# Optimization experiments

Measured on AMD Instinct MI355X. Metric: run time of the kernel, lower is better.

The kernel has to match this reference:

```python
import jax, jax.numpy as jnp
import numpy as np


def lut_quantize(v, lut):
    """Nearest-neighbor LUT quantization with straight-through estimator.
    lut is sorted ascending; uses searchsorted (no [N, L] blowup)."""
    L = lut.shape[0]
    idx = jnp.clip(jnp.searchsorted(lut, v), 1, L - 1)
    left = jnp.take(lut, idx - 1)
    right = jnp.take(lut, idx)
    q = jnp.where(v - left <= right - v, left, right)
    return v + jax.lax.stop_gradient(q - v)


def mem_conv(x, w, b, lut):
    # memConv2d: weights/bias snapped to LUT levels, then standard 3x3 SAME conv (NCHW/OIHW)
    wq = lut_quantize(w, lut)
    bq = lut_quantize(b, lut)
    y = jax.lax.conv_general_dilated(x, wq, window_strides=(1, 1),
                                     padding=((1, 1), (1, 1)),
                                     dimension_numbers=('NCHW', 'OIHW', 'NCHW'))
    return y + bq[None, :, None, None]


def mem_linear(x, w, b, lut):
    # memLinear: torch-style weight (out, in)
    return x @ lut_quantize(w, lut).T + lut_quantize(b, lut)


def mem_relu(x, lut):
    # memReLu: ReLU followed by LUT quantization of the activation
    return lut_quantize(jnp.maximum(x, 0.0), lut)


def max_pool_2x2(x):
    return jax.lax.reduce_window(x, -jnp.inf, jax.lax.max,
                                 (1, 1, 2, 2), (1, 1, 2, 2), 'VALID')


def _forward(x, lut, w1, b1, w2, b2, w3, b3, w4, b4, w5, b5, w6, b6,
             fw1, fb1, fw2, fb2, fw3, fb3):
    x = mem_relu(mem_conv(x, w1, b1, lut), lut)
    x = mem_relu(mem_conv(x, w2, b2, lut), lut)
    x = max_pool_2x2(x)                      # [B,32,16,16]
    x = mem_relu(mem_conv(x, w3, b3, lut), lut)
    x = mem_relu(mem_conv(x, w4, b4, lut), lut)
    x = max_pool_2x2(x)                      # [B,64,8,8]
    x = mem_relu(mem_conv(x, w5, b5, lut), lut)
    x = mem_relu(mem_conv(x, w6, b6, lut), lut)
    x = max_pool_2x2(x)                      # [B,128,4,4]
    x = x.reshape(-1, 128 * 4 * 4)
    x = mem_relu(mem_linear(x, fw1, fb1, lut), lut)
    x = mem_relu(mem_linear(x, fw2, fb2, lut), lut)
    x = mem_linear(x, fw3, fb3, lut)
    return jax.nn.softmax(x, axis=1)


def setup_inputs() -> dict:
    key = jax.random.key(0)
    ks = jax.random.split(key, 20)
    B = 512
    lut = jnp.linspace(-4.0, 4.0, 129).astype(jnp.float32)

    def conv_w(k, co, ci):
        scale = np.sqrt(2.0 / (ci * 9)).astype(np.float32)
        return jax.random.normal(k, (co, ci, 3, 3), jnp.float32) * scale

    def lin_w(k, co, ci):
        scale = np.sqrt(2.0 / ci).astype(np.float32)
        return jax.random.normal(k, (co, ci), jnp.float32) * scale

    return {
        'x': jax.random.normal(ks[0], (B, 3, 32, 32), jnp.float32),
        'lut': lut,
        'w1': conv_w(ks[1], 32, 3),   'b1': jnp.zeros((32,), jnp.float32),
        'w2': conv_w(ks[2], 32, 32),  'b2': jnp.zeros((32,), jnp.float32),
        'w3': conv_w(ks[3], 64, 32),  'b3': jnp.zeros((64,), jnp.float32),
        'w4': conv_w(ks[4], 64, 64),  'b4': jnp.zeros((64,), jnp.float32),
        'w5': conv_w(ks[5], 128, 64), 'b5': jnp.zeros((128,), jnp.float32),
        'w6': conv_w(ks[6], 128, 128),'b6': jnp.zeros((128,), jnp.float32),
        'fw1': lin_w(ks[7], 512, 2048), 'fb1': jnp.zeros((512,), jnp.float32),
        'fw2': lin_w(ks[8], 128, 512),  'fb2': jnp.zeros((128,), jnp.float32),
        'fw3': lin_w(ks[9], 10, 128),   'fb3': jnp.zeros((10,), jnp.float32),
    }


def reference(x, lut, w1, b1, w2, b2, w3, b3, w4, b4, w5, b5, w6, b6,
              fw1, fb1, fw2, fb2, fw3, fb3):
    return _forward(x, lut, w1, b1, w2, b2, w3, b3, w4, b4, w5, b5, w6, b6,
                    fw1, fb1, fw2, fb2, fw3, fb3)
```

## Files before the change

### kernel.cpp

```cpp
#include <hip/hip_runtime.h>
#include <cstddef>


#define B_SZ 512
typedef unsigned int u32;
typedef __attribute__((ext_vector_type(4))) int i32x4;

__device__ __forceinline__ float lutq(float v) {
    float k = ceilf(v * 16.0f - 0.5f);
    k = fminf(64.0f, fmaxf(-64.0f, k));
    return k * 0.0625f;
}
__device__ __forceinline__ int kq(float x) {
    float kf = ceilf(x * 16.0f - 0.5f);
    kf = fminf(64.0f, fmaxf(-64.0f, kf));
    return (int)kf;
}
__device__ __forceinline__ u32 bmax4u(u32 a, u32 b) {
    u32 r = 0;
    #pragma unroll
    for (int j = 0; j < 4; ++j) {
        u32 x = (a >> (8 * j)) & 255u, y = (b >> (8 * j)) & 255u;
        r |= (x > y ? x : y) << (8 * j);
    }
    return r;
}

__device__ __forceinline__ void prep_conv_frag(const float* __restrict__ w, char* __restrict__ q,
                                               int i, int CI) {
    int NSTEP = (9 * CI + 63) / 64;
    int e = i & 15, t = i >> 4;
    int ln = t & 63, t2 = t >> 6;
    int s = t2 % NSTEP, co_tile = t2 / NSTEP;
    int k = s * 64 + ((ln >> 4) << 4) + e;
    int tap = k / CI, ci = k % CI;
    int co = co_tile * 16 + (ln & 15);
    int val = 0;
    if (tap < 9) val = kq(w[(co * CI + ci) * 9 + tap]);
    q[i] = (char)val;
}
__device__ __forceinline__ void prep_fc_frag(const float* __restrict__ w, char* __restrict__ q,
                                             int i, int K) {
    int S = K >> 6;
    int e = i & 15, t = i >> 4;
    int ln = t & 63, t2 = t >> 6;
    int s = t2 % S, n_tile = t2 / S;
    int n = n_tile * 16 + (ln & 15);
    int k = s * 64 + ((ln >> 4) << 4) + e;
    q[i] = (char)kq(w[(size_t)n * K + k]);
}

__global__ __launch_bounds__(256) void prep_conv1(
    const float* __restrict__ w2, const float* __restrict__ w3, const float* __restrict__ w4,
    const float* __restrict__ w5, const float* __restrict__ w6,
    const float* __restrict__ fw1, const float* __restrict__ fw2,
    char* q2, char* q3, char* q4, char* q5, char* q6, char* qf1, char* qf2,
    const float* __restrict__ x, const float* __restrict__ w1,
    const float* __restrict__ b1, char* __restrict__ out)
{
    const int tid = threadIdx.x;
    const int bid = blockIdx.x;
    if (bid < 5480) {
        int i = bid * 256 + tid;
        if (i < 10240)                  { prep_conv_frag(w2, q2, i, 32);  }
        else if ((i -= 10240) < 20480)  { prep_conv_frag(w3, q3, i, 32);  }
        else if ((i -= 20480) < 36864)  { prep_conv_frag(w4, q4, i, 64);  }
        else if ((i -= 36864) < 73728)  { prep_conv_frag(w5, q5, i, 64);  }
        else if ((i -= 73728) < 147456) { prep_conv_frag(w6, q6, i, 128); }
        else if ((i -= 147456) < 1048576){ prep_fc_frag(fw1, qf1, i, 2048); }
        else if ((i -= 1048576) < 65536) { prep_fc_frag(fw2, qf2, i, 512);  }
        return;
    }
    __shared__ float s_w[3][9][32];
    __shared__ float s_b[32];
    __shared__ float s_in[3][10][34];
    const int bx  = bid - 5480;
    const int b   = bx >> 2;
    const int r0  = (bx & 3) * 8;
    for (int i = tid; i < 864; i += 256) {
        int o = i % 32, k = (i / 32) % 9, c = i / 288;
        s_w[c][k][o] = lutq(w1[(o * 3 + c) * 9 + k]);
    }
    if (tid < 32) s_b[tid] = lutq(b1[tid]);
    for (int i = tid; i < 3 * 10 * 34; i += 256) {
        int xx = i % 34, yy = (i / 34) % 10, c = i / 340;
        int gy = r0 + yy - 1, gx = xx - 1;
        float v = 0.f;
        if ((unsigned)gy < 32u && (unsigned)gx < 32u)
            v = x[(((size_t)b * 3 + c) * 32 + gy) * 32 + gx];
        s_in[c][yy][xx] = v;
    }
    __syncthreads();
    const int y = tid >> 5, xx = tid & 31;
    float acc[32];
    #pragma unroll
    for (int o = 0; o < 32; ++o) acc[o] = 0.f;
    #pragma unroll
    for (int c = 0; c < 3; ++c) {
        #pragma unroll
        for (int k = 0; k < 9; ++k) {
            float iv = s_in[c][y + k / 3][xx + k % 3];
            #pragma unroll
            for (int o = 0; o < 32; ++o) acc[o] = fmaf(iv, s_w[c][k][o], acc[o]);
        }
    }
    u32 u[8];
    #pragma unroll
    for (int j = 0; j < 8; ++j) {
        u32 p = 0;
        #pragma unroll
        for (int q = 0; q < 4; ++q) {
            float v = fmaxf(acc[4 * j + q] + s_b[4 * j + q], 0.f);
            int kk = (int)ceilf(v * 16.0f - 0.5f);
            kk = kk > 64 ? 64 : kk;
            p |= ((u32)kk & 255u) << (8 * q);
        }
        u[j] = p;
    }
    const int p = (b << 10) + ((r0 + y) << 5) + xx;
    u32* o4 = (u32*)(out + (size_t)p * 32);
    #pragma unroll
    for (int j = 0; j < 8; ++j) o4[j] = u[j];
}

template<int HW, int CI, int CO, int RS, int NIMG, int NT, int POOL = 0>
__global__ __launch_bounds__(256) void conv_mfma(
    const char* __restrict__ in,
    const char* __restrict__ wq,
    const float* __restrict__ bias,
    char* __restrict__ out)
{
    constexpr int PH  = HW + 2;
    constexpr int PIX = NIMG * (RS + 2) * PH;
    constexpr int M   = NIMG * RS * HW;
    constexpr int MT  = M / 16;
    constexpr int MW  = MT / 4;
    constexpr int NSTEP = (9 * CI + 63) / 64;
    constexpr int SL  = HW / RS;
    constexpr int NC16 = CI / 16;
    constexpr int NTC = NT * 16;

    __shared__ __align__(128) char s_in[PIX * CI];

    const int tid = threadIdx.x;
    const int g   = blockIdx.x;
    const int b0  = (g / SL) * NIMG;
    const int r0  = (g % SL) * RS;
    const int co0 = blockIdx.y * NTC;

    constexpr int TOTC = PIX * NC16;
    for (int i = tid; i < TOTC; i += 256) {
        int c16 = i % NC16;
        int pp  = i / NC16;
        int xx  = pp % PH;
        int rr  = pp / PH;
        int yy  = rr % (RS + 2);
        int img = rr / (RS + 2);
        int gy = r0 + yy - 1, gx = xx - 1;
        uint4 v = {0u, 0u, 0u, 0u};
        if ((unsigned)gy < (unsigned)HW && (unsigned)gx < (unsigned)HW)
            v = *(const uint4*)(in + ((((size_t)(b0 + img) * HW + gy) * HW + gx) * CI + c16 * 16));
        int off = (pp * CI + c16 * 16) ^ ((pp & 7) << 4);
        *(uint4*)(s_in + off) = v;
    }
    __syncthreads();

    const int wv = tid >> 6, ln = tid & 63;
    const int l15 = ln & 15, lq = ln >> 4;

    int ppad[MW];
    #pragma unroll
    for (int mw = 0; mw < MW; ++mw) {
        int p = (wv * MW + mw) * 16 + l15;
        int img = p / (RS * HW);
        int rem = p % (RS * HW);
        int ly = rem / HW, lx = rem % HW;
        ppad[mw] = (img * (RS + 2) + ly + 1) * PH + lx + 1;
    }

    i32x4 acc[MW][NT] = {};

    const char* wtile = wq + ((size_t)blockIdx.y * NT) * NSTEP * 1024 + (ln << 4);
    auto dp = [](int t) { return (t / 3 - 1) * PH + (t % 3 - 1); };

    #pragma unroll
    for (int s = 0; s < NSTEP; ++s) {
        i32x4 bf[NT];
        #pragma unroll
        for (int nt = 0; nt < NT; ++nt)
            bf[nt] = *(const i32x4*)(wtile + ((nt * NSTEP + s) << 10));
        int dd, ci0;
        if constexpr (CI == 32) {
            int d0 = dp(2 * s);
            int d1 = (2 * s + 1 < 9) ? dp(2 * s + 1) : 0;
            dd  = (lq & 2) ? d1 : d0;
            ci0 = (lq & 1) << 4;
        } else if constexpr (CI == 64) {
            dd  = dp(s);
            ci0 = lq << 4;
        } else {
            dd  = dp(s >> 1);
            ci0 = ((s & 1) << 6) + (lq << 4);
        }
        #pragma unroll
        for (int mw = 0; mw < MW; ++mw) {
            int pix = ppad[mw] + dd;
            int off = (pix * CI + ci0) ^ ((pix & 7) << 4);
            i32x4 af = *(const i32x4*)(s_in + off);
            #pragma unroll
            for (int nt = 0; nt < NT; ++nt)
                acc[mw][nt] = __builtin_amdgcn_mfma_i32_16x16x64_i8(af, bf[nt], acc[mw][nt], 0, 0, 0);
        }
    }

    if constexpr (POOL == 0) {
        #pragma unroll
        for (int nt = 0; nt < NT; ++nt) {
            int kb16 = 16 * kq(bias[co0 + nt * 16 + l15]);
            #pragma unroll
            for (int mw = 0; mw < MW; ++mw) {
                #pragma unroll
                for (int r = 0; r < 4; ++r) {
                    int p = (wv * MW + mw) * 16 + lq * 4 + r;
                    int img = p / (RS * HW), rem = p % (RS * HW);
                    int ly = rem / HW, lx = rem % HW;
                    int vv = acc[mw][nt][r] + kb16;
                    vv = vv > 0 ? vv : 0;
                    int kk = (vv + 7) >> 4;
                    kk = kk > 64 ? 64 : kk;
                    out[(((size_t)(b0 + img) * HW + r0 + ly) * HW + lx) * CO + co0 + nt * 16 + l15] = (char)kk;
                }
            }
        }
    } else {
        __syncthreads();
        char* s_out = s_in;
        #pragma unroll
        for (int nt = 0; nt < NT; ++nt) {
            int kb16 = 16 * kq(bias[co0 + nt * 16 + l15]);
            #pragma unroll
            for (int mw = 0; mw < MW; ++mw) {
                #pragma unroll
                for (int r = 0; r < 4; ++r) {
                    int p = (wv * MW + mw) * 16 + lq * 4 + r;
                    int vv = acc[mw][nt][r] + kb16;
                    vv = vv > 0 ? vv : 0;
                    int kk = (vv + 7) >> 4;
                    kk = kk > 64 ? 64 : kk;
                    s_out[p * NTC + nt * 16 + l15] = (char)kk;
                }
            }
        }
        __syncthreads();
        constexpr int PR = RS / 2, PC = HW / 2, HOW = HW / 2;
        constexpr int OCT = NIMG * PR * PC * (NTC / 16);
        for (int idx = tid; idx < OCT; idx += 256) {
            int c16 = idx % (NTC / 16);
            int pp  = idx / (NTC / 16);
            int xo = pp % PC, yo = (pp / PC) % PR, img = pp / (PC * PR);
            int pb = (img * RS + 2 * yo) * HW + 2 * xo;
            uint4 v0 = *(const uint4*)(s_out + (pb)          * NTC + c16 * 16);
            uint4 v1 = *(const uint4*)(s_out + (pb + 1)      * NTC + c16 * 16);
            uint4 v2 = *(const uint4*)(s_out + (pb + HW)     * NTC + c16 * 16);
            uint4 v3 = *(const uint4*)(s_out + (pb + HW + 1) * NTC + c16 * 16);
            uint4 r;
            r.x = bmax4u(bmax4u(v0.x, v1.x), bmax4u(v2.x, v3.x));
            r.y = bmax4u(bmax4u(v0.y, v1.y), bmax4u(v2.y, v3.y));
            r.z = bmax4u(bmax4u(v0.z, v1.z), bmax4u(v2.z, v3.z));
            r.w = bmax4u(bmax4u(v0.w, v1.w), bmax4u(v2.w, v3.w));
            if constexpr (POOL == 1) {
                *(uint4*)(out + ((((size_t)(b0 + img) * HOW + (r0 >> 1) + yo) * HOW + xo) * CO
                                 + co0 + c16 * 16)) = r;
            } else {
                const char* rv = (const char*)&r;
                int m = b0 + img;
                #pragma unroll
                for (int j = 0; j < 16; ++j) {
                    int c = co0 + c16 * 16 + j;
                    int k = c * 16 + yo * 4 + xo;
                    int off = (((m >> 4) * 32 + (k >> 6)) << 10)
                            + ((((k >> 4) & 3) * 16 + (m & 15)) << 4) + (k & 15);
                    out[off] = rv[j];
                }
            }
        }
    }
}

template<int N, int K, int SK>
__global__ __launch_bounds__(256) void fc1_splitk(
    const char* __restrict__ xa, const char* __restrict__ wq, int* __restrict__ part)
{
    constexpr int KCH = K / SK;
    constexpr int KS = K / 64;
    const int tid = threadIdx.x, wv = tid >> 6, ln = tid & 63;
    const int l15 = ln & 15, lq = ln >> 4;
    const int m0 = blockIdx.x * 128, n0 = blockIdx.y * 128;
    const int kb = blockIdx.z * KCH;
    const int mq = (wv >> 1) * 4, nq = (wv & 1) * 4;
    i32x4 acc[4][4] = {};
    const char* xr[4];
    const char* wt[4];
    #pragma unroll
    for (int t = 0; t < 4; ++t) {
        xr[t] = xa + (size_t)((m0 >> 4) + mq + t) * KS * 1024 + (ln << 4);
        wt[t] = wq + (size_t)((n0 >> 4) + nq + t) * KS * 1024 + (ln << 4);
    }
    for (int k0 = 0; k0 < KCH; k0 += 64) {
        const int s = (kb + k0) >> 6;
        i32x4 a[4], b[4];
        #pragma unroll
        for (int t = 0; t < 4; ++t) {
            a[t] = *(const i32x4*)(xr[t] + (s << 10));
            b[t] = *(const i32x4*)(wt[t] + (s << 10));
        }
        #pragma unroll
        for (int i = 0; i < 4; ++i)
            #pragma unroll
            for (int j = 0; j < 4; ++j)
                acc[i][j] = __builtin_amdgcn_mfma_i32_16x16x64_i8(a[i], b[j], acc[i][j], 0, 0, 0);
    }
    int* pb = part + (size_t)blockIdx.z * (B_SZ * N);
    #pragma unroll
    for (int j = 0; j < 4; ++j) {
        int n = n0 + (nq + j) * 16 + l15;
        #pragma unroll
        for (int i = 0; i < 4; ++i)
            #pragma unroll
            for (int r = 0; r < 4; ++r) {
                int m = m0 + (mq + i) * 16 + lq * 4 + r;
                pb[(size_t)m * N + n] = acc[i][j][r];
            }
    }
}

template<int N, int SK>
__global__ __launch_bounds__(256) void fc_reduce(
    const int* __restrict__ part, const float* __restrict__ bias, char* __restrict__ out)
{
    int i = blockIdx.x * 256 + threadIdx.x;
    if (i >= B_SZ * N) return;
    int s = 0;
    #pragma unroll
    for (int k = 0; k < SK; ++k) s += part[(size_t)k * (B_SZ * N) + i];
    int vv = s + 16 * kq(bias[i % N]);
    vv = vv > 0 ? vv : 0;
    int kk = (vv + 7) >> 4;
    kk = kk > 64 ? 64 : kk;
    out[i] = (char)kk;
}

__global__ __launch_bounds__(256) void fc_tail(
    const char* __restrict__ x, const char* __restrict__ qf2,
    const float* __restrict__ fb2, const float* __restrict__ fw3,
    const float* __restrict__ fb3, float* __restrict__ out)
{
    __shared__ __align__(16) char sx[16 * 512];
    __shared__ __align__(16) char sy[16 * 128];
    __shared__ __align__(16) char sw3[10 * 128];
    __shared__ float sb3[10];
    __shared__ int sp[16][16][10];

    const int tid = threadIdx.x;
    const int m0 = blockIdx.x * 16;

    for (int idx = tid; idx < 512; idx += 256) {
        int r = idx >> 5, c16 = idx & 31;
        uint4 v = *(const uint4*)(x + (size_t)(m0 + r) * 512 + c16 * 16);
        *(uint4*)(sx + ((r * 512 + c16 * 16) ^ ((r & 7) << 4))) = v;
    }
    for (int i = tid; i < 1280; i += 256) sw3[i] = (char)kq(fw3[i]);
    if (tid < 10) sb3[tid] = lutq(fb3[tid]);
    __syncthreads();

    const int wv = tid >> 6, ln = tid & 63, l15 = ln & 15, lq = ln >> 4;
    const int ntg = wv * 2;
    i32x4 acc[2] = {};
    #pragma unroll
    for (int s = 0; s < 8; ++s) {
        int row = l15;
        i32x4 a = *(const i32x4*)(sx + ((row * 512 + s * 64 + lq * 16) ^ ((row & 7) << 4)));
        #pragma unroll
        for (int nt = 0; nt < 2; ++nt) {
            i32x4 b = *(const i32x4*)(qf2 + (((ntg + nt) * 8 + s) << 10) + (ln << 4));
            acc[nt] = __builtin_amdgcn_mfma_i32_16x16x64_i8(a, b, acc[nt], 0, 0, 0);
        }
    }
    #pragma unroll
    for (int nt = 0; nt < 2; ++nt) {
        int n = (ntg + nt) * 16 + l15;
        int kb16 = 16 * kq(fb2[n]);
        #pragma unroll
        for (int r = 0; r < 4; ++r) {
            int row = lq * 4 + r;
            int vv = acc[nt][r] + kb16;
            vv = vv > 0 ? vv : 0;
            int kk = (vv + 7) >> 4;
            kk = kk > 64 ? 64 : kk;
            sy[(row * 128 + n) ^ ((row & 7) << 4)] = (char)kk;
        }
    }
    __syncthreads();

    {
        int r = tid >> 4, g = tid & 15;
        uint2 yv = *(const uint2*)(sy + ((r * 128 + g * 8) ^ ((r & 7) << 4)));
        const char* yb = (const char*)&yv;
        #pragma unroll
        for (int o = 0; o < 10; ++o) {
            uint2 wv2 = *(const uint2*)(sw3 + o * 128 + g * 8);
            const char* wb = (const char*)&wv2;
            int S = 0;
            #pragma unroll
            for (int e = 0; e < 8; ++e) S += (int)yb[e] * (int)wb[e];
            sp[r][g][o] = S;
        }
    }
    __syncthreads();

    if (tid < 16) {
        int r = tid;
        float d[10];
        #pragma unroll
        for (int o = 0; o < 10; ++o) {
            int S = 0;
            #pragma unroll
            for (int g = 0; g < 16; ++g) S += sp[r][g][o];
            d[o] = (float)S * 0.00390625f + sb3[o];
        }
        float m = d[0];
        #pragma unroll
        for (int o = 1; o < 10; ++o) m = fmaxf(m, d[o]);
        float e[10];
        float sum = 0.f;
        #pragma unroll
        for (int o = 0; o < 10; ++o) { e[o] = expf(d[o] - m); sum += e[o]; }
        #pragma unroll
        for (int o = 0; o < 10; ++o) out[(size_t)(m0 + r) * 10 + o] = e[o] / sum;
    }
}

extern "C" void kernel_launch(void* const* d_in, const int* in_sizes, int n_in,
                              void* d_out, int out_size, void* d_ws, size_t ws_size,
                              hipStream_t stream)
{
    const float* x   = (const float*)d_in[0];
    const float* w1  = (const float*)d_in[2];
    const float* b1  = (const float*)d_in[3];
    const float* w2  = (const float*)d_in[4];
    const float* b2  = (const float*)d_in[5];
    const float* w3  = (const float*)d_in[6];
    const float* b3  = (const float*)d_in[7];
    const float* w4  = (const float*)d_in[8];
    const float* b4  = (const float*)d_in[9];
    const float* w5  = (const float*)d_in[10];
    const float* b5  = (const float*)d_in[11];
    const float* w6  = (const float*)d_in[12];
    const float* b6  = (const float*)d_in[13];
    const float* fw1 = (const float*)d_in[14];
    const float* fb1 = (const float*)d_in[15];
    const float* fw2 = (const float*)d_in[16];
    const float* fb2 = (const float*)d_in[17];
    const float* fw3 = (const float*)d_in[18];
    const float* fb3 = (const float*)d_in[19];
    float* out = (float*)d_out;

    char* bufA = (char*)d_ws;
    char* bufB = bufA + (16u << 20);
    char* q2  = bufB + (16u << 20);
    char* q3  = q2 + 10240;
    char* q4  = q3 + 20480;
    char* q5  = q4 + 36864;
    char* q6  = q5 + 73728;
    char* qf1 = q6 + 147456;
    char* qf2 = qf1 + 1048576;
    int*  part = (int*)(qf2 + 65536);
    char* fc1out = (char*)part + (16u << 20);
    char* fc1a   = fc1out + 262144;

    dim3 blk(256);

    prep_conv1<<<dim3(7528), blk, 0, stream>>>(
        w2, w3, w4, w5, w6, fw1, fw2, q2, q3, q4, q5, q6, qf1, qf2,
        x, w1, b1, bufA);
    conv_mfma<32, 32, 32, 8, 1, 2, 1><<<dim3(2048, 1), blk, 0, stream>>>(bufA, q2, b2, bufB);
    conv_mfma<16, 32, 64, 8, 1, 4, 0><<<dim3(1024, 1), blk, 0, stream>>>(bufB, q3, b3, bufA);
    conv_mfma<16, 64, 64, 8, 1, 4, 1><<<dim3(1024, 1), blk, 0, stream>>>(bufA, q4, b4, bufB);
    conv_mfma<8, 64, 128, 8, 1, 4, 0><<<dim3(512, 2), blk, 0, stream>>>(bufB, q5, b5, bufA);
    conv_mfma<8, 128, 128, 8, 1, 4, 2><<<dim3(512, 2), blk, 0, stream>>>(bufA, q6, b6, fc1a);
    fc1_splitk<512, 2048, 16><<<dim3(4, 4, 16), blk, 0, stream>>>(fc1a, qf1, part);
    fc_reduce<512, 16><<<dim3(1024), blk, 0, stream>>>(part, fb1, fc1out);
    fc_tail<<<dim3(32), blk, 0, stream>>>(fc1out, qf2, fb2, fw3, fb3, out);
}
```

Baseline: 96.55 us.

## Fuse conv3+conv4 and conv5+conv6 pairs into per-image kernels with shared-memory intermediates

Replaces four generic conv_mfma launches with two fused kernels, each processing one image per block. conv3's output (and conv5's) is kept in padded, swizzled shared memory and fed straight into conv4 (conv6), so the global-memory round trip and two launches are removed. Each block now holds a whole image, which may lower occupancy: 512 blocks, and conv56 runs only one 16-row M tile per wave with 8 N tiles. A requant helper is also factored out for readability.

```diff
diff --git a/kernel.cpp b/kernel.cpp
--- a/kernel.cpp
+++ b/kernel.cpp
@@ -24,6 +24,12 @@
         r |= (x > y ? x : y) << (8 * j);
     }
     return r;
+}
+__device__ __forceinline__ int requant(int s, int kb16) {
+    int vv = s + kb16;
+    vv = vv > 0 ? vv : 0;
+    int kk = (vv + 7) >> 4;
+    return kk > 64 ? 64 : kk;
 }
 
 __device__ __forceinline__ void prep_conv_frag(const float* __restrict__ w, char* __restrict__ q,
@@ -125,10 +131,8 @@
 
 template<int HW, int CI, int CO, int RS, int NIMG, int NT, int POOL = 0>
 __global__ __launch_bounds__(256) void conv_mfma(
-    const char* __restrict__ in,
-    const char* __restrict__ wq,
-    const float* __restrict__ bias,
-    char* __restrict__ out)
+    const char* __restrict__ in, const char* __restrict__ wq,
+    const float* __restrict__ bias, char* __restrict__ out)
 {
     constexpr int PH  = HW + 2;
     constexpr int PIX = NIMG * (RS + 2) * PH;
@@ -179,7 +183,6 @@
     }
 
     i32x4 acc[MW][NT] = {};
-
     const char* wtile = wq + ((size_t)blockIdx.y * NT) * NSTEP * 1024 + (ln << 4);
     auto dp = [](int t) { return (t / 3 - 1) * PH + (t % 3 - 1); };
 
@@ -218,19 +221,15 @@
         for (int nt = 0; nt < NT; ++nt) {
             int kb16 = 16 * kq(bias[co0 + nt * 16 + l15]);
             #pragma unroll
-            for (int mw = 0; mw < MW; ++mw) {
+            for (int mw = 0; mw < MW; ++mw)
                 #pragma unroll
                 for (int r = 0; r < 4; ++r) {
                     int p = (wv * MW + mw) * 16 + lq * 4 + r;
                     int img = p / (RS * HW), rem = p % (RS * HW);
                     int ly = rem / HW, lx = rem % HW;
-                    int vv = acc[mw][nt][r] + kb16;
-                    vv = vv > 0 ? vv : 0;
-                    int kk = (vv + 7) >> 4;
-                    kk = kk > 64 ? 64 : kk;
-                    out[(((size_t)(b0 + img) * HW + r0 + ly) * HW + lx) * CO + co0 + nt * 16 + l15] = (char)kk;
+                    out[(((size_t)(b0 + img) * HW + r0 + ly) * HW + lx) * CO + co0 + nt * 16 + l15] =
+                        (char)requant(acc[mw][nt][r], kb16);
                 }
-            }
         }
     } else {
         __syncthreads();
@@ -239,17 +238,12 @@
         for (int nt = 0; nt < NT; ++nt) {
             int kb16 = 16 * kq(bias[co0 + nt * 16 + l15]);
             #pragma unroll
-            for (int mw = 0; mw < MW; ++mw) {
+            for (int mw = 0; mw < MW; ++mw)
                 #pragma unroll
                 for (int r = 0; r < 4; ++r) {
                     int p = (wv * MW + mw) * 16 + lq * 4 + r;
-                    int vv = acc[mw][nt][r] + kb16;
-                    vv = vv > 0 ? vv : 0;
-                    int kk = (vv + 7) >> 4;
-                    kk = kk > 64 ? 64 : kk;
-                    s_out[p * NTC + nt * 16 + l15] = (char)kk;
+                    s_out[p * NTC + nt * 16 + l15] = (char)requant(acc[mw][nt][r], kb16);
                 }
-            }
         }
         __syncthreads();
         constexpr int PR = RS / 2, PC = HW / 2, HOW = HW / 2;
@@ -268,21 +262,243 @@
             r.y = bmax4u(bmax4u(v0.y, v1.y), bmax4u(v2.y, v3.y));
             r.z = bmax4u(bmax4u(v0.z, v1.z), bmax4u(v2.z, v3.z));
             r.w = bmax4u(bmax4u(v0.w, v1.w), bmax4u(v2.w, v3.w));
-            if constexpr (POOL == 1) {
-                *(uint4*)(out + ((((size_t)(b0 + img) * HOW + (r0 >> 1) + yo) * HOW + xo) * CO
-                                 + co0 + c16 * 16)) = r;
-            } else {
-                const char* rv = (const char*)&r;
-                int m = b0 + img;
-                #pragma unroll
-                for (int j = 0; j < 16; ++j) {
-                    int c = co0 + c16 * 16 + j;
-                    int k = c * 16 + yo * 4 + xo;
-                    int off = (((m >> 4) * 32 + (k >> 6)) << 10)
-                            + ((((k >> 4) & 3) * 16 + (m & 15)) << 4) + (k & 15);
-                    out[off] = rv[j];
-                }
+            *(uint4*)(out + ((((size_t)(b0 + img) * HOW + (r0 >> 1) + yo) * HOW + xo) * CO
+                             + co0 + c16 * 16)) = r;
+        }
+    }
+}
+
+__global__ __launch_bounds__(256) void conv34(
+    const char* __restrict__ in,
+    const char* __restrict__ q3, const float* __restrict__ b3,
+    const char* __restrict__ q4, const float* __restrict__ b4,
+    char* __restrict__ out)
+{
+    __shared__ __align__(128) char s_in[18 * 18 * 32];
+    __shared__ __align__(128) char mid[18 * 18 * 64];
+    const int tid = threadIdx.x;
+    const int b   = blockIdx.x;
+    const int wv = tid >> 6, ln = tid & 63, l15 = ln & 15, lq = ln >> 4;
+
+    for (int i = tid; i < 648; i += 256) {
+        int c16 = i & 1;
+        int pp  = i >> 1;
+        int xx = pp % 18, yy = pp / 18;
+        int gy = yy - 1, gx = xx - 1;
+        uint4 v = {0u, 0u, 0u, 0u};
+        if ((unsigned)gy < 16u && (unsigned)gx < 16u)
+            v = *(const uint4*)(in + (((size_t)b * 16 + gy) * 16 + gx) * 32 + c16 * 16);
+        int off = (pp * 32 + c16 * 16) ^ ((pp & 7) << 4);
+        *(uint4*)(s_in + off) = v;
+    }
+    for (int i = tid; i < 5184; i += 256) ((u32*)mid)[i] = 0u;
+    __syncthreads();
+
+    int ppad[4];
+    #pragma unroll
+    for (int mw = 0; mw < 4; ++mw) {
+        int p = (wv * 4 + mw) * 16 + l15;
+        ppad[mw] = ((p >> 4) + 1) * 18 + (p & 15) + 1;
+    }
+    auto dp18 = [](int t) { return (t / 3 - 1) * 18 + (t % 3 - 1); };
+
+    i32x4 acc3[4][4] = {};
+    #pragma unroll
+    for (int s = 0; s < 5; ++s) {
+        i32x4 bf[4];
+        #pragma unroll
+        for (int nt = 0; nt < 4; ++nt)
+            bf[nt] = *(const i32x4*)(q3 + ((nt * 5 + s) << 10) + (ln << 4));
+        int d0 = dp18(2 * s);
+        int d1 = (2 * s + 1 < 9) ? dp18(2 * s + 1) : 0;
+        int dd = (lq & 2) ? d1 : d0;
+        int ci0 = (lq & 1) << 4;
+        #pragma unroll
+        for (int mw = 0; mw < 4; ++mw) {
+            int pix = ppad[mw] + dd;
+            int off = (pix * 32 + ci0) ^ ((pix & 7) << 4);
+            i32x4 af = *(const i32x4*)(s_in + off);
+            #pragma unroll
+            for (int nt = 0; nt < 4; ++nt)
+                acc3[mw][nt] = __builtin_amdgcn_mfma_i32_16x16x64_i8(af, bf[nt], acc3[mw][nt], 0, 0, 0);
+        }
+    }
+    #pragma unroll
+    for (int nt = 0; nt < 4; ++nt) {
+        int kb16 = 16 * kq(b3[nt * 16 + l15]);
+        #pragma unroll
+        for (int mw = 0; mw < 4; ++mw)
+            #pragma unroll
+            for (int r = 0; r < 4; ++r) {
+                int p = (wv * 4 + mw) * 16 + lq * 4 + r;
+                int pix = ((p >> 4) + 1) * 18 + (p & 15) + 1;
+                mid[(pix * 64 + nt * 16 + l15) ^ ((pix & 7) << 4)] =
+                    (char)requant(acc3[mw][nt][r], kb16);
             }
+    }
+    __syncthreads();
+
+    i32x4 acc4[4][4] = {};
+    #pragma unroll
+    for (int s = 0; s < 9; ++s) {
+        i32x4 bf[4];
+        #pragma unroll
+        for (int nt = 0; nt < 4; ++nt)
+            bf[nt] = *(const i32x4*)(q4 + ((nt * 9 + s) << 10) + (ln << 4));
+        int dd = dp18(s);
+        int ci0 = lq << 4;
+        #pragma unroll
+        for (int mw = 0; mw < 4; ++mw) {
+            int pix = ppad[mw] + dd;
+            int off = (pix * 64 + ci0) ^ ((pix & 7) << 4);
+            i32x4 af = *(const i32x4*)(mid + off);
+            #pragma unroll
+            for (int nt = 0; nt < 4; ++nt)
+                acc4[mw][nt] = __builtin_amdgcn_mfma_i32_16x16x64_i8(af, bf[nt], acc4[mw][nt], 0, 0, 0);
+        }
+    }
+    __syncthreads();
+    char* s_out = mid;
+    #pragma unroll
+    for (int nt = 0; nt < 4; ++nt) {
+        int kb16 = 16 * kq(b4[nt * 16 + l15]);
+        #pragma unroll
+        for (int mw = 0; mw < 4; ++mw)
+            #pragma unroll
+            for (int r = 0; r < 4; ++r) {
+                int p = (wv * 4 + mw) * 16 + lq * 4 + r;
+                s_out[p * 64 + nt * 16 + l15] = (char)requant(acc4[mw][nt][r], kb16);
+            }
+    }
+    __syncthreads();
+    {
+        int c16 = tid & 3;
+        int pp  = tid >> 2;
+        int xo = pp & 7, yo = pp >> 3;
+        int pb = (2 * yo) * 16 + 2 * xo;
+        uint4 v0 = *(const uint4*)(s_out + (pb)      * 64 + c16 * 16);
+        uint4 v1 = *(const uint4*)(s_out + (pb + 1)  * 64 + c16 * 16);
+        uint4 v2 = *(const uint4*)(s_out + (pb + 16) * 64 + c16 * 16);
+        uint4 v3 = *(const uint4*)(s_out + (pb + 17) * 64 + c16 * 16);
+        uint4 r;
+        r.x = bmax4u(bmax4u(v0.x, v1.x), bmax4u(v2.x, v3.x));
+        r.y = bmax4u(bmax4u(v0.y, v1.y), bmax4u(v2.y, v3.y));
+        r.z = bmax4u(bmax4u(v0.z, v1.z), bmax4u(v2.z, v3.z));
+        r.w = bmax4u(bmax4u(v0.w, v1.w), bmax4u(v2.w, v3.w));
+        *(uint4*)(out + (((size_t)b * 8 + yo) * 8 + xo) * 64 + c16 * 16) = r;
+    }
+}
+
+__global__ __launch_bounds__(256) void conv56(
+    const char* __restrict__ in,
+    const char* __restrict__ q5, const float* __restrict__ b5,
+    const char* __restrict__ q6, const float* __restrict__ b6,
+    char* __restrict__ fc1a)
+{
+    __shared__ __align__(128) char sA[8192];
+    __shared__ __align__(128) char sB[12800];
+    const int tid = threadIdx.x;
+    const int b   = blockIdx.x;
+    const int wv = tid >> 6, ln = tid & 63, l15 = ln & 15, lq = ln >> 4;
+
+    for (int i = tid; i < 400; i += 256) {
+        int c16 = i & 3;
+        int pp  = i >> 2;
+        int xx = pp % 10, yy = pp / 10;
+        int gy = yy - 1, gx = xx - 1;
+        uint4 v = {0u, 0u, 0u, 0u};
+        if ((unsigned)gy < 8u && (unsigned)gx < 8u)
+            v = *(const uint4*)(in + (((size_t)b * 8 + gy) * 8 + gx) * 64 + c16 * 16);
+        int off = (pp * 64 + c16 * 16) ^ ((pp & 7) << 4);
+        *(uint4*)(sA + off) = v;
+    }
+    for (int i = tid; i < 3200; i += 256) ((u32*)sB)[i] = 0u;
+    __syncthreads();
+
+    const int p0 = wv * 16 + l15;
+    const int ppad = ((p0 >> 3) + 1) * 10 + (p0 & 7) + 1;
+    auto dp10 = [](int t) { return (t / 3 - 1) * 10 + (t % 3 - 1); };
+
+    i32x4 acc5[8] = {};
+    #pragma unroll
+    for (int s = 0; s < 9; ++s) {
+        i32x4 bf[8];
+        #pragma unroll
+        for (int nt = 0; nt < 8; ++nt)
+            bf[nt] = *(const i32x4*)(q5 + ((nt * 9 + s) << 10) + (ln << 4));
+        int dd = dp10(s);
+        int ci0 = lq << 4;
+        int pix = ppad + dd;
+        int off = (pix * 64 + ci0) ^ ((pix & 7) << 4);
+        i32x4 af = *(const i32x4*)(sA + off);
+        #pragma unroll
+        for (int nt = 0; nt < 8; ++nt)
+            acc5[nt] = __builtin_amdgcn_mfma_i32_16x16x64_i8(af, bf[nt], acc5[nt], 0, 0, 0);
+    }
+    #pragma unroll
+    for (int nt = 0; nt < 8; ++nt) {
+        int kb16 = 16 * kq(b5[nt * 16 + l15]);
+        #pragma unroll
+        for (int r = 0; r < 4; ++r) {
+            int p = wv * 16 + lq * 4 + r;
+            int pix = ((p >> 3) + 1) * 10 + (p & 7) + 1;
+            sB[(pix * 128 + nt * 16 + l15) ^ ((pix & 7) << 4)] =
+                (char)requant(acc5[nt][r], kb16);
+        }
+    }
+    __syncthreads();
+
+    i32x4 acc6[8] = {};
+    #pragma unroll
+    for (int s = 0; s < 18; ++s) {
+        i32x4 bf[8];
+        #pragma unroll
+        for (int nt = 0; nt < 8; ++nt)
+            bf[nt] = *(const i32x4*)(q6 + ((nt * 18 + s) << 10) + (ln << 4));
+        int dd = dp10(s >> 1);
+        int ci0 = ((s & 1) << 6) + (lq << 4);
+        int pix = ppad + dd;
+        int off = (pix * 128 + ci0) ^ ((pix & 7) << 4);
+        i32x4 af = *(const i32x4*)(sB + off);
+        #pragma unroll
+        for (int nt = 0; nt < 8; ++nt)
+            acc6[nt] = __builtin_amdgcn_mfma_i32_16x16x64_i8(af, bf[nt], acc6[nt], 0, 0, 0);
+    }
+    __syncthreads();
+    char* s_out = sA;
+    #pragma unroll
+    for (int nt = 0; nt < 8; ++nt) {
+        int kb16 = 16 * kq(b6[nt * 16 + l15]);
+        #pragma unroll
+        for (int r = 0; r < 4; ++r) {
+            int p = wv * 16 + lq * 4 + r;
+            s_out[p * 128 + nt * 16 + l15] = (char)requant(acc6[nt][r], kb16);
+        }
+    }
+    __syncthreads();
+    if (tid < 128) {
+        int c16 = tid & 7;
+        int pp  = tid >> 3;
+        int xo = pp & 3, yo = pp >> 2;
+        int pb = (2 * yo) * 8 + 2 * xo;
+        uint4 v0 = *(const uint4*)(s_out + (pb)     * 128 + c16 * 16);
+        uint4 v1 = *(const uint4*)(s_out + (pb + 1) * 128 + c16 * 16);
+        uint4 v2 = *(const uint4*)(s_out + (pb + 8) * 128 + c16 * 16);
+        uint4 v3 = *(const uint4*)(s_out + (pb + 9) * 128 + c16 * 16);
+        uint4 r;
+        r.x = bmax4u(bmax4u(v0.x, v1.x), bmax4u(v2.x, v3.x));
+        r.y = bmax4u(bmax4u(v0.y, v1.y), bmax4u(v2.y, v3.y));
+        r.z = bmax4u(bmax4u(v0.z, v1.z), bmax4u(v2.z, v3.z));
+        r.w = bmax4u(bmax4u(v0.w, v1.w), bmax4u(v2.w, v3.w));
+        const char* rv = (const char*)&r;
+        int m = b;
+        #pragma unroll
+        for (int j = 0; j < 16; ++j) {
+            int c = c16 * 16 + j;
+            int k = c * 16 + yo * 4 + xo;
+            int off = (((m >> 4) * 32 + (k >> 6)) << 10)
+                    + ((((k >> 4) & 3) * 16 + (m & 15)) << 4) + (k & 15);
+            fc1a[off] = rv[j];
         }
     }
 }
@@ -343,11 +559,7 @@
     int s = 0;
     #pragma unroll
     for (int k = 0; k < SK; ++k) s += part[(size_t)k * (B_SZ * N) + i];
-    int vv = s + 16 * kq(bias[i % N]);
-    vv = vv > 0 ? vv : 0;
-    int kk = (vv + 7) >> 4;
-    kk = kk > 64 ? 64 : kk;
-    out[i] = (char)kk;
+    out[i] = (char)requant(s, 16 * kq(bias[i % N]));
 }
 
 __global__ __launch_bounds__(256) void fc_tail(
@@ -393,11 +605,7 @@
         #pragma unroll
         for (int r = 0; r < 4; ++r) {
             int row = lq * 4 + r;
-            int vv = acc[nt][r] + kb16;
-            vv = vv > 0 ? vv : 0;
-            int kk = (vv + 7) >> 4;
-            kk = kk > 64 ? 64 : kk;
-            sy[(row * 128 + n) ^ ((row & 7) << 4)] = (char)kk;
+            sy[(row * 128 + n) ^ ((row & 7) << 4)] = (char)requant(acc[nt][r], kb16);
         }
     }
     __syncthreads();
@@ -484,10 +692,8 @@
         w2, w3, w4, w5, w6, fw1, fw2, q2, q3, q4, q5, q6, qf1, qf2,
         x, w1, b1, bufA);
     conv_mfma<32, 32, 32, 8, 1, 2, 1><<<dim3(2048, 1), blk, 0, stream>>>(bufA, q2, b2, bufB);
-    conv_mfma<16, 32, 64, 8, 1, 4, 0><<<dim3(1024, 1), blk, 0, stream>>>(bufB, q3, b3, bufA);
-    conv_mfma<16, 64, 64, 8, 1, 4, 1><<<dim3(1024, 1), blk, 0, stream>>>(bufA, q4, b4, bufB);
-    conv_mfma<8, 64, 128, 8, 1, 4, 0><<<dim3(512, 2), blk, 0, stream>>>(bufB, q5, b5, bufA);
-    conv_mfma<8, 128, 128, 8, 1, 4, 2><<<dim3(512, 2), blk, 0, stream>>>(bufA, q6, b6, fc1a);
+    conv34<<<dim3(512), blk, 0, stream>>>(bufB, q3, b3, q4, b4, bufA);
+    conv56<<<dim3(512), blk, 0, stream>>>(bufA, q5, b5, q6, b6, fc1a);
     fc1_splitk<512, 2048, 16><<<dim3(4, 4, 16), blk, 0, stream>>>(fc1a, qf1, part);
     fc_reduce<512, 16><<<dim3(1024), blk, 0, stream>>>(part, fb1, fc1out);
     fc_tail<<<dim3(32), blk, 0, stream>>>(fc1out, qf2, fb2, fw3, fb3, out);
```

After: 97.43 us. No clear change (+0.9%).
